# Optimization experiments

Hardware: AMD Instinct MI355X
Metric: run time of the kernel (lower is better)

The kernel has to match this reference:

```python
import jax, jax.numpy as jnp
import numpy as np

B, T, D, E, F, K = 1, 8192, 1024, 8, 4096, 2
CAP_FACTOR = 1.25
AUX_COEFF = 0.01


def setup_inputs() -> dict:
    key = jax.random.key(0)
    k0, k1, k2, k3, k4 = jax.random.split(key, 5)
    x = jax.random.normal(k0, (B, T, D), dtype=jnp.float32)
    Wr = jax.random.normal(k1, (E, D), dtype=jnp.float32) * 0.01  # router, std=0.01 per init
    s = 0.02
    Wg = jax.random.normal(k2, (E, F, D), dtype=jnp.float32) * s  # gate_proj per expert
    Wu = jax.random.normal(k3, (E, F, D), dtype=jnp.float32) * s  # up_proj per expert
    Wd = jax.random.normal(k4, (E, D, F), dtype=jnp.float32) * s  # down_proj per expert
    return {"x": x, "Wr": Wr, "Wg": Wg, "Wu": Wu, "Wd": Wd}


def reference(x, Wr, Wg, Wu, Wd):
    b, t, d = x.shape
    N = b * t
    capacity = max(int(t * K * CAP_FACTOR / E), 1)  # static, matches compute_capacity
    x_flat = x.reshape(N, d)

    # --- router ---
    logits = x_flat @ Wr.T                              # (N, E)
    probs = jax.nn.softmax(logits, axis=-1)
    topw_raw, topi = jax.lax.top_k(probs, K)            # (N, K)
    topw = topw_raw / (topw_raw.sum(-1, keepdims=True) + 1e-9)

    # --- dispatch order: slot-major (slot 0 over all tokens, then slot 1, ...) ---
    flat_e = topi.T.reshape(-1)                         # (K*N,) expert id per assignment
    flat_w = topw.T.reshape(-1)                         # (K*N,)
    tok = jnp.tile(jnp.arange(N), K)                    # (K*N,) token id per assignment

    oh = jax.nn.one_hot(flat_e, E, dtype=jnp.int32)     # (K*N, E)
    rank = (jnp.cumsum(oh, axis=0) - oh)[jnp.arange(K * N), flat_e]  # arrival rank per expert
    accepted = rank < capacity                          # dispatch_mask (slot-major flat)
    pos = jnp.where(accepted, rank, 0)
    dest = flat_e * capacity + pos                      # slot in flattened capacity buffer
    acc_f = accepted.astype(x.dtype)[:, None]

    # scatter tokens into capacity buffers (dropped tokens add zeros)
    buf = jnp.zeros((E * capacity, d), x.dtype).at[dest].add(x_flat[tok] * acc_f)
    expert_in = buf.reshape(E, capacity, d)

    # --- per-expert SwiGLU FFN (batched grouped GEMM) ---
    gate = jax.nn.silu(jnp.einsum('ecd,efd->ecf', expert_in, Wg))
    up = jnp.einsum('ecd,efd->ecf', expert_in, Wu)
    expert_out = jnp.einsum('ecf,edf->ecd', gate * up, Wd).reshape(E * capacity, d)

    # --- weighted combine back to token positions ---
    contrib = flat_w[:, None] * acc_f * expert_out[dest]
    out_flat = jnp.zeros((N, d), x.dtype).at[tok].add(contrib)
    output = out_flat.reshape(b, t, d)

    # --- load-balance aux loss ---
    counts = jnp.zeros(E, x.dtype).at[flat_e].add(accepted.astype(x.dtype))
    total = jnp.maximum(accepted.sum().astype(x.dtype), 1.0)
    f_i = counts / total
    P_i = probs.mean(0)
    aux_loss = AUX_COEFF * E * jnp.sum(f_i * P_i)
    return output, aux_loss
```

## Files before the change

### kernel.cpp

```cpp
#include <hip/hip_runtime.h>
#include <hip/hip_bf16.h>

#define N_TOK 8192
#define DIM   1024
#define NEXP  8
#define FF    4096
#define CAP   2560
#define NASSIGN (N_TOK * 2)

typedef __bf16 bf16;
typedef __bf16 bf16x8 __attribute__((ext_vector_type(8)));
typedef __bf16 bf16x4v __attribute__((ext_vector_type(4)));
typedef float  f32x4  __attribute__((ext_vector_type(4)));

__device__ __forceinline__ void gl2lds16(const bf16* g, bf16* l) {
    __builtin_amdgcn_global_load_lds(
        (const __attribute__((address_space(1))) unsigned int*)g,
        (__attribute__((address_space(3))) unsigned int*)l,
        16, 0, 0);
}

template <int NT>
__device__ __forceinline__ void gemm256_core(
    const bf16* __restrict__ gA, size_t astep,
    const bf16* __restrict__ gB, size_t bstep,
    bf16* As, bf16* Bs, f32x4 acc[8][4], int wave, int lane)
{
    const int wm = wave >> 2, wn = wave & 3;
    const int r16 = lane & 15, c16 = lane >> 4;

    auto STAGE = [&](int kt) {
        const int b = kt & 1;
        const bf16* a  = gA + kt * 64;
        const bf16* bb = gB + kt * 64;
#pragma unroll
        for (int g = 0; g < 4; ++g)
            gl2lds16(a + (size_t)g * astep, &As[b * (256 * 64) + (g * 64 + wave * 8) * 64]);
#pragma unroll
        for (int g = 0; g < 4; ++g)
            gl2lds16(bb + (size_t)g * bstep, &Bs[b * (256 * 64) + (g * 64 + wave * 8) * 64]);
    };

    STAGE(0);
    STAGE(1);

    bf16x8 af[4][2], bfr[2][2];

    for (int kt = 0; kt < NT; ++kt) {
        if (kt < NT - 1) asm volatile("s_waitcnt vmcnt(8)" ::: "memory");
        else             asm volatile("s_waitcnt vmcnt(0)" ::: "memory");
        __builtin_amdgcn_sched_barrier(0);
        __builtin_amdgcn_s_barrier();
        __builtin_amdgcn_sched_barrier(0);
        const bf16* Asb = &As[(kt & 1) * (256 * 64)];
        const bf16* Bsb = &Bs[(kt & 1) * (256 * 64)];

#define DS_A(mh)                                                          \
        _Pragma("unroll")                                                 \
        for (int m = 0; m < 4; ++m) {                                     \
            _Pragma("unroll")                                             \
            for (int kk = 0; kk < 2; ++kk) {                              \
                int row = wm * 128 + (mh) * 64 + m * 16 + r16;            \
                int phys = (kk * 4 + c16) ^ (row & 7);                    \
                af[m][kk] = *(const bf16x8*)&Asb[row * 64 + phys * 8];    \
            } }
#define DS_B(nh)                                                          \
        _Pragma("unroll")                                                 \
        for (int n = 0; n < 2; ++n) {                                     \
            _Pragma("unroll")                                             \
            for (int kk = 0; kk < 2; ++kk) {                              \
                int row = wn * 64 + ((nh) * 2 + n) * 16 + r16;            \
                int phys = (kk * 4 + c16) ^ (row & 7);                    \
                bfr[n][kk] = *(const bf16x8*)&Bsb[row * 64 + phys * 8];   \
            } }
#define PH_IN                                                             \
        __builtin_amdgcn_sched_barrier(0);                                \
        __builtin_amdgcn_s_barrier();                                     \
        asm volatile("s_waitcnt lgkmcnt(0)" ::: "memory");                \
        __builtin_amdgcn_sched_barrier(0);
#define PH_MFMA(mh, nh)                                                   \
        __builtin_amdgcn_s_setprio(1);                                    \
        _Pragma("unroll")                                                 \
        for (int m = 0; m < 4; ++m)                                       \
            _Pragma("unroll")                                             \
            for (int n = 0; n < 2; ++n)                                   \
                _Pragma("unroll")                                         \
                for (int kk = 0; kk < 2; ++kk)                            \
                    acc[(mh) * 4 + m][(nh) * 2 + n] =                     \
                        __builtin_amdgcn_mfma_f32_16x16x32_bf16(          \
                            af[m][kk], bfr[n][kk],                        \
                            acc[(mh) * 4 + m][(nh) * 2 + n], 0, 0, 0);    \
        __builtin_amdgcn_s_setprio(0);
#define PH_OUT                                                            \
        __builtin_amdgcn_sched_barrier(0);                                \
        __builtin_amdgcn_s_barrier();                                     \
        __builtin_amdgcn_sched_barrier(0);

        DS_A(0) DS_B(0) PH_IN PH_MFMA(0, 0) PH_OUT
        DS_B(1)         PH_IN PH_MFMA(0, 1) PH_OUT
        DS_A(1) DS_B(0) PH_IN PH_MFMA(1, 0) PH_OUT
        DS_B(1)         PH_IN PH_MFMA(1, 1) PH_OUT

#undef DS_A
#undef DS_B
#undef PH_IN
#undef PH_MFMA
#undef PH_OUT

        if (kt + 2 < NT) STAGE(kt + 2);
    }
}

__global__ __launch_bounds__(256) void cvt_bf16_kernel(const float* __restrict__ in,
                                                       bf16* __restrict__ out, int n) {
    int stride = gridDim.x * blockDim.x * 8;
    for (int i = (blockIdx.x * blockDim.x + threadIdx.x) * 8; i < n; i += stride) {
        float4 a = *(const float4*)(in + i);
        float4 b = *(const float4*)(in + i + 4);
        bf16x8 o;
        o[0] = (bf16)a.x; o[1] = (bf16)a.y; o[2] = (bf16)a.z; o[3] = (bf16)a.w;
        o[4] = (bf16)b.x; o[5] = (bf16)b.y; o[6] = (bf16)b.z; o[7] = (bf16)b.w;
        *(bf16x8*)(out + i) = o;
    }
}

__global__ __launch_bounds__(256) void router_kernel(const float* __restrict__ x,
                                                     const float* __restrict__ Wr,
                                                     float* __restrict__ probs,
                                                     int* __restrict__ topi,
                                                     float* __restrict__ topw) {
    int wave = threadIdx.x >> 6;
    int lane = threadIdx.x & 63;
    int t = blockIdx.x * 4 + wave;
    const float* xr = x + (size_t)t * DIM;

    double acc[NEXP];
#pragma unroll
    for (int e = 0; e < NEXP; ++e) acc[e] = 0.0;
    for (int i = lane; i < DIM; i += 64) {
        double xv = (double)xr[i];
#pragma unroll
        for (int e = 0; e < NEXP; ++e) acc[e] += xv * (double)Wr[e * DIM + i];
    }
#pragma unroll
    for (int e = 0; e < NEXP; ++e) {
        double v = acc[e];
        for (int off = 32; off > 0; off >>= 1) v += __shfl_down(v, off, 64);
        acc[e] = v;
    }
    if (lane == 0) {
        double mx = acc[0];
        for (int e = 1; e < NEXP; ++e) if (acc[e] > mx) mx = acc[e];
        double p[NEXP], s = 0.0;
        for (int e = 0; e < NEXP; ++e) { p[e] = exp(acc[e] - mx); s += p[e]; }
        float pf[NEXP];
        for (int e = 0; e < NEXP; ++e) { pf[e] = (float)(p[e] / s); probs[t * NEXP + e] = pf[e]; }
        int e1 = 0;
        for (int e = 1; e < NEXP; ++e) if (acc[e] > acc[e1]) e1 = e;
        int e2 = -1;
        for (int e = 0; e < NEXP; ++e) {
            if (e == e1) continue;
            if (e2 < 0 || acc[e] > acc[e2]) e2 = e;
        }
        float w1 = pf[e1], w2 = pf[e2];
        float inv = 1.0f / (w1 + w2 + 1e-9f);
        topi[t * 2 + 0] = e1; topi[t * 2 + 1] = e2;
        topw[t * 2 + 0] = w1 * inv; topw[t * 2 + 1] = w2 * inv;
    }
}

__global__ __launch_bounds__(64) void rank_kernel(const int* __restrict__ topi,
                                                  int* __restrict__ dest,
                                                  int* __restrict__ accf,
                                                  int* __restrict__ counts) {
    int e = blockIdx.x;
    int lane = threadIdx.x;
    const int per = NASSIGN / 64;
    int base = lane * per;
    int cnt = 0;
    for (int i = 0; i < per; ++i) {
        int j = base + i;
        int t = j & (N_TOK - 1), s = j >> 13;
        if (topi[t * 2 + s] == e) cnt++;
    }
    int sum = cnt;
    for (int off = 1; off < 64; off <<= 1) {
        int v = __shfl_up(sum, off, 64);
        if (lane >= off) sum += v;
    }
    int r = sum - cnt;
    int total = __shfl(sum, 63, 64);
    for (int i = 0; i < per; ++i) {
        int j = base + i;
        int t = j & (N_TOK - 1), s = j >> 13;
        if (topi[t * 2 + s] == e) {
            int acc = (r < CAP) ? 1 : 0;
            dest[j] = e * CAP + (acc ? r : 0);
            accf[j] = acc;
            r++;
        }
    }
    if (lane == 63) counts[e] = (total < CAP) ? total : CAP;
}

__global__ __launch_bounds__(256) void gather_kernel(const float* __restrict__ x,
                                                     const int* __restrict__ dest,
                                                     const int* __restrict__ accf,
                                                     bf16* __restrict__ Xe) {
    int j = blockIdx.x;
    if (!accf[j]) return;
    int t = j & (N_TOK - 1);
    int d0 = threadIdx.x * 4;
    float4 v = *(const float4*)(x + (size_t)t * DIM + d0);
    union { bf16 h[4]; uint2 u; } tmp;
    tmp.h[0] = (bf16)v.x; tmp.h[1] = (bf16)v.y; tmp.h[2] = (bf16)v.z; tmp.h[3] = (bf16)v.w;
    *(uint2*)(Xe + (size_t)dest[j] * DIM + d0) = tmp.u;
}

__global__ __launch_bounds__(512, 2) void gateup_kernel(const bf16* __restrict__ Xe,
                                                        const bf16* __restrict__ Wg,
                                                        const bf16* __restrict__ Wu,
                                                        bf16* __restrict__ hbuf) {
    const int e = blockIdx.z;
    const int m0 = blockIdx.x * 256;
    const int n0f = blockIdx.y * 128;
    const int tid = threadIdx.x, lane = tid & 63, wave = tid >> 6;
    const int wm = wave >> 2, wn = wave & 3;
    const int r16 = lane & 15, c16 = lane >> 4;

    __shared__ bf16 As[2 * 256 * 64];
    __shared__ bf16 Bs[2 * 256 * 64];

    const int rsub = wave * 8 + (lane >> 3);
    const int csw  = ((lane & 7) ^ (lane >> 3)) * 8;
    const bf16* gA = Xe + (size_t)e * CAP * DIM + (size_t)(m0 + rsub) * DIM + csw;
    const int bff = n0f + ((rsub >> 5) & 1) * 16 + (rsub & 15);
    const bf16* gB = (((rsub >> 4) & 1) ? Wu : Wg)
                   + (size_t)e * FF * DIM + (size_t)bff * DIM + csw;

    f32x4 acc[8][4] = {};
    gemm256_core<DIM / 64>(gA, (size_t)64 * DIM, gB, (size_t)32 * DIM, As, Bs, acc, wave, lane);

    bf16* hp = hbuf + (size_t)e * CAP * FF;
#pragma unroll
    for (int m = 0; m < 8; ++m)
#pragma unroll
        for (int np = 0; np < 2; ++np)
#pragma unroll
            for (int j = 0; j < 4; ++j) {
                float g = acc[m][2 * np + 0][j];
                float u = acc[m][2 * np + 1][j];
                float h = (g / (1.f + __expf(-g))) * u;
                int gr = m0 + wm * 128 + m * 16 + c16 * 4 + j;
                int gc = n0f + wn * 32 + np * 16 + r16;
                hp[(size_t)gr * FF + gc] = (bf16)h;
            }
}

__global__ __launch_bounds__(512, 2) void down_kernel(const bf16* __restrict__ hbuf,
                                                      const bf16* __restrict__ Wd,
                                                      bf16* __restrict__ eo) {
    const int e  = blockIdx.z >> 1;
    const int kh = blockIdx.z & 1;
    const int m0 = blockIdx.x * 256;
    const int n0 = blockIdx.y * 256;
    const int tid = threadIdx.x, lane = tid & 63, wave = tid >> 6;
    const int wm = wave >> 2, wn = wave & 3;
    const int r16 = lane & 15, c16 = lane >> 4;

    __shared__ bf16 As[2 * 256 * 64];
    __shared__ bf16 Bs[2 * 256 * 64];

    const int rsub = wave * 8 + (lane >> 3);
    const int csw  = ((lane & 7) ^ (lane >> 3)) * 8;
    const bf16* gA = hbuf + (size_t)e * CAP * FF + (size_t)(m0 + rsub) * FF + kh * (FF / 2) + csw;
    const bf16* gB = Wd + (size_t)e * DIM * FF + (size_t)(n0 + rsub) * FF + kh * (FF / 2) + csw;

    f32x4 acc[8][4] = {};
    gemm256_core<FF / 128>(gA, (size_t)64 * FF, gB, (size_t)64 * FF, As, Bs, acc, wave, lane);

    bf16* op = eo + (size_t)kh * NEXP * CAP * DIM + (size_t)e * CAP * DIM;
#pragma unroll
    for (int m = 0; m < 8; ++m)
#pragma unroll
        for (int n = 0; n < 4; ++n)
#pragma unroll
            for (int j = 0; j < 4; ++j) {
                int gr = m0 + wm * 128 + m * 16 + c16 * 4 + j;
                int gc = n0 + wn * 64 + n * 16 + r16;
                op[(size_t)gr * DIM + gc] = (bf16)acc[m][n][j];
            }
}

__global__ __launch_bounds__(256) void combine_kernel(const bf16* __restrict__ eo,
                                                      const int* __restrict__ dest,
                                                      const int* __restrict__ accf,
                                                      const float* __restrict__ topw,
                                                      float* __restrict__ out) {
    int t = blockIdx.x;
    float w0 = accf[t] ? topw[t * 2 + 0] : 0.f;
    float w1 = accf[N_TOK + t] ? topw[t * 2 + 1] : 0.f;
    size_t off1 = (size_t)NEXP * CAP * DIM;
    const bf16* a0 = eo + (size_t)dest[t] * DIM;
    const bf16* b0 = eo + (size_t)dest[N_TOK + t] * DIM;
    int d = threadIdx.x * 4;
    bf16x4v a00 = *(const bf16x4v*)(a0 + d);
    bf16x4v a01 = *(const bf16x4v*)(a0 + off1 + d);
    bf16x4v b00 = *(const bf16x4v*)(b0 + d);
    bf16x4v b01 = *(const bf16x4v*)(b0 + off1 + d);
    float4 o;
    o.x = w0 * ((float)a00[0] + (float)a01[0]) + w1 * ((float)b00[0] + (float)b01[0]);
    o.y = w0 * ((float)a00[1] + (float)a01[1]) + w1 * ((float)b00[1] + (float)b01[1]);
    o.z = w0 * ((float)a00[2] + (float)a01[2]) + w1 * ((float)b00[2] + (float)b01[2]);
    o.w = w0 * ((float)a00[3] + (float)a01[3]) + w1 * ((float)b00[3] + (float)b01[3]);
    *(float4*)(out + (size_t)t * DIM + d) = o;
}

__global__ __launch_bounds__(256) void aux_kernel(const float* __restrict__ probs,
                                                  const int* __restrict__ counts,
                                                  float* __restrict__ out_aux) {
    __shared__ float sm[256][NEXP];
    float loc[NEXP];
#pragma unroll
    for (int e = 0; e < NEXP; ++e) loc[e] = 0.f;
    for (int t = threadIdx.x; t < N_TOK; t += 256)
#pragma unroll
        for (int e = 0; e < NEXP; ++e) loc[e] += probs[t * NEXP + e];
#pragma unroll
    for (int e = 0; e < NEXP; ++e) sm[threadIdx.x][e] = loc[e];
    __syncthreads();
    for (int s = 128; s > 0; s >>= 1) {
        if (threadIdx.x < s)
#pragma unroll
            for (int e = 0; e < NEXP; ++e) sm[threadIdx.x][e] += sm[threadIdx.x + s][e];
        __syncthreads();
    }
    if (threadIdx.x == 0) {
        int tot = 0;
        for (int e = 0; e < NEXP; ++e) tot += counts[e];
        float totf = tot > 0 ? (float)tot : 1.f;
        float aux = 0.f;
        for (int e = 0; e < NEXP; ++e)
            aux += ((float)counts[e] / totf) * (sm[0][e] / (float)N_TOK);
        out_aux[0] = 0.01f * (float)NEXP * aux;
    }
}

extern "C" void kernel_launch(void* const* d_in, const int* in_sizes, int n_in,
                              void* d_out, int out_size, void* d_ws, size_t ws_size,
                              hipStream_t stream) {
    const float* x  = (const float*)d_in[0];
    const float* Wr = (const float*)d_in[1];
    const float* Wg = (const float*)d_in[2];
    const float* Wu = (const float*)d_in[3];
    const float* Wd = (const float*)d_in[4];
    float* out = (float*)d_out;

    char* ws = (char*)d_ws;
    size_t off = 0;
    auto alloc = [&](size_t bytes) -> void* {
        void* p = ws + off;
        off += (bytes + 255) & ~(size_t)255;
        return p;
    };
    const size_t NW = (size_t)NEXP * FF * DIM;
    bf16*  Wg_bf = (bf16*)alloc(NW * sizeof(bf16));
    bf16*  Wu_bf = (bf16*)alloc(NW * sizeof(bf16));
    bf16*  Wd_bf = (bf16*)alloc(NW * sizeof(bf16));
    bf16*  Xe    = (bf16*)alloc((size_t)NEXP * CAP * DIM * sizeof(bf16));
    bf16*  hbuf  = (bf16*)alloc((size_t)NEXP * CAP * FF * sizeof(bf16));
    bf16*  eo    = (bf16*)alloc((size_t)2 * NEXP * CAP * DIM * sizeof(bf16));
    float* probs = (float*)alloc((size_t)N_TOK * NEXP * sizeof(float));
    int*   topi  = (int*)alloc((size_t)N_TOK * 2 * sizeof(int));
    float* topw  = (float*)alloc((size_t)N_TOK * 2 * sizeof(float));
    int*   dst   = (int*)alloc((size_t)NASSIGN * sizeof(int));
    int*   accf  = (int*)alloc((size_t)NASSIGN * sizeof(int));
    int*   cnts  = (int*)alloc(NEXP * sizeof(int));

    cvt_bf16_kernel<<<2048, 256, 0, stream>>>(Wg, Wg_bf, (int)NW);
    cvt_bf16_kernel<<<2048, 256, 0, stream>>>(Wu, Wu_bf, (int)NW);
    cvt_bf16_kernel<<<2048, 256, 0, stream>>>(Wd, Wd_bf, (int)NW);
    router_kernel<<<N_TOK / 4, 256, 0, stream>>>(x, Wr, probs, topi, topw);
    rank_kernel<<<NEXP, 64, 0, stream>>>(topi, dst, accf, cnts);
    gather_kernel<<<NASSIGN, 256, 0, stream>>>(x, dst, accf, Xe);
    gateup_kernel<<<dim3(CAP / 256, FF / 128, NEXP), 512, 0, stream>>>(Xe, Wg_bf, Wu_bf, hbuf);
    down_kernel<<<dim3(CAP / 256, DIM / 256, NEXP * 2), 512, 0, stream>>>(hbuf, Wd_bf, eo);
    combine_kernel<<<N_TOK, 256, 0, stream>>>(eo, dst, accf, topw, out);
    aux_kernel<<<1, 256, 0, stream>>>(probs, cnts, out + (size_t)N_TOK * DIM);
}
```

Before: 1.024 ms.

## Interleave global-to-LDS prefetch into MFMA phases with quarter-tile staging

```diff
diff --git a/kernel.cpp b/kernel.cpp
--- a/kernel.cpp
+++ b/kernel.cpp
@@ -20,95 +20,105 @@
         16, 0, 0);
 }
 
-template <int NT>
+template <int NT, int AST, int BST, int BG1, int BG2>
 __device__ __forceinline__ void gemm256_core(
-    const bf16* __restrict__ gA, size_t astep,
-    const bf16* __restrict__ gB, size_t bstep,
+    const bf16* __restrict__ pA, const bf16* __restrict__ pB,
     bf16* As, bf16* Bs, f32x4 acc[8][4], int wave, int lane)
 {
     const int wm = wave >> 2, wn = wave & 3;
     const int r16 = lane & 15, c16 = lane >> 4;
-
-    auto STAGE = [&](int kt) {
-        const int b = kt & 1;
-        const bf16* a  = gA + kt * 64;
-        const bf16* bb = gB + kt * 64;
-#pragma unroll
-        for (int g = 0; g < 4; ++g)
-            gl2lds16(a + (size_t)g * astep, &As[b * (256 * 64) + (g * 64 + wave * 8) * 64]);
-#pragma unroll
-        for (int g = 0; g < 4; ++g)
-            gl2lds16(bb + (size_t)g * bstep, &Bs[b * (256 * 64) + (g * 64 + wave * 8) * 64]);
-    };
-
-    STAGE(0);
-    STAGE(1);
+    const int wbase = wave * 8 * 64;
+
+#define AOFF(g) ((size_t)(g) * 64 * AST)
+#define BOFF(g) ((size_t)(((g) & 1) * BG1 + ((g) >> 1) * BG2) * BST)
+#define SA(g, kt) gl2lds16(pA + AOFF(g) + (size_t)(kt) * 64, \
+                           &As[((kt) & 1) * (256 * 64) + (g) * (64 * 64) + wbase])
+#define SB(g, kt) gl2lds16(pB + BOFF(g) + (size_t)(kt) * 64, \
+                           &Bs[((kt) & 1) * (256 * 64) + (g) * (64 * 64) + wbase])
+
+    SA(0, 0); SA(2, 0); SB(0, 0); SB(1, 0);
+    SA(1, 0); SA(3, 0); SB(2, 0); SB(3, 0);
+    SA(0, 1); SA(2, 1); SB(0, 1); SB(1, 1);
+    asm volatile("s_waitcnt vmcnt(4)" ::: "memory");
+    __builtin_amdgcn_sched_barrier(0);
+    __builtin_amdgcn_s_barrier();
+    __builtin_amdgcn_sched_barrier(0);
 
     bf16x8 af[4][2], bfr[2][2];
 
-    for (int kt = 0; kt < NT; ++kt) {
-        if (kt < NT - 1) asm volatile("s_waitcnt vmcnt(8)" ::: "memory");
-        else             asm volatile("s_waitcnt vmcnt(0)" ::: "memory");
-        __builtin_amdgcn_sched_barrier(0);
-        __builtin_amdgcn_s_barrier();
-        __builtin_amdgcn_sched_barrier(0);
-        const bf16* Asb = &As[(kt & 1) * (256 * 64)];
-        const bf16* Bsb = &Bs[(kt & 1) * (256 * 64)];
-
-#define DS_A(mh)                                                          \
-        _Pragma("unroll")                                                 \
-        for (int m = 0; m < 4; ++m) {                                     \
-            _Pragma("unroll")                                             \
-            for (int kk = 0; kk < 2; ++kk) {                              \
-                int row = wm * 128 + (mh) * 64 + m * 16 + r16;            \
-                int phys = (kk * 4 + c16) ^ (row & 7);                    \
-                af[m][kk] = *(const bf16x8*)&Asb[row * 64 + phys * 8];    \
-            } }
-#define DS_B(nh)                                                          \
-        _Pragma("unroll")                                                 \
-        for (int n = 0; n < 2; ++n) {                                     \
-            _Pragma("unroll")                                             \
-            for (int kk = 0; kk < 2; ++kk) {                              \
-                int row = wn * 64 + ((nh) * 2 + n) * 16 + r16;            \
-                int phys = (kk * 4 + c16) ^ (row & 7);                    \
-                bfr[n][kk] = *(const bf16x8*)&Bsb[row * 64 + phys * 8];   \
-            } }
-#define PH_IN                                                             \
-        __builtin_amdgcn_sched_barrier(0);                                \
-        __builtin_amdgcn_s_barrier();                                     \
-        asm volatile("s_waitcnt lgkmcnt(0)" ::: "memory");                \
-        __builtin_amdgcn_sched_barrier(0);
-#define PH_MFMA(mh, nh)                                                   \
-        __builtin_amdgcn_s_setprio(1);                                    \
-        _Pragma("unroll")                                                 \
-        for (int m = 0; m < 4; ++m)                                       \
-            _Pragma("unroll")                                             \
-            for (int n = 0; n < 2; ++n)                                   \
-                _Pragma("unroll")                                         \
-                for (int kk = 0; kk < 2; ++kk)                            \
-                    acc[(mh) * 4 + m][(nh) * 2 + n] =                     \
-                        __builtin_amdgcn_mfma_f32_16x16x32_bf16(          \
-                            af[m][kk], bfr[n][kk],                        \
-                            acc[(mh) * 4 + m][(nh) * 2 + n], 0, 0, 0);    \
-        __builtin_amdgcn_s_setprio(0);
-#define PH_OUT                                                            \
-        __builtin_amdgcn_sched_barrier(0);                                \
-        __builtin_amdgcn_s_barrier();                                     \
-        __builtin_amdgcn_sched_barrier(0);
-
-        DS_A(0) DS_B(0) PH_IN PH_MFMA(0, 0) PH_OUT
-        DS_B(1)         PH_IN PH_MFMA(0, 1) PH_OUT
-        DS_A(1) DS_B(0) PH_IN PH_MFMA(1, 0) PH_OUT
-        DS_B(1)         PH_IN PH_MFMA(1, 1) PH_OUT
-
+#define DS_A(mh)                                                           \
+    _Pragma("unroll")                                                      \
+    for (int mm = 0; mm < 4; ++mm) {                                       \
+        _Pragma("unroll")                                                  \
+        for (int kk = 0; kk < 2; ++kk) {                                   \
+            int row = wm * 128 + (mh) * 64 + mm * 16 + r16;                \
+            int phys = (kk * 4 + c16) ^ (row & 7);                         \
+            af[mm][kk] = *(const bf16x8*)&Asb[row * 64 + phys * 8];        \
+        } }
+#define DS_B(nh)                                                           \
+    _Pragma("unroll")                                                      \
+    for (int np = 0; np < 2; ++np) {                                       \
+        _Pragma("unroll")                                                  \
+        for (int kk = 0; kk < 2; ++kk) {                                   \
+            int rl = (nh) * 128 + wn * 32 + np * 16 + r16;                 \
+            int phys = (kk * 4 + c16) ^ (rl & 7);                          \
+            bfr[np][kk] = *(const bf16x8*)&Bsb[rl * 64 + phys * 8];        \
+        } }
+#define PH_IN                                                              \
+    __builtin_amdgcn_sched_barrier(0);                                     \
+    __builtin_amdgcn_s_barrier();                                          \
+    asm volatile("s_waitcnt lgkmcnt(0)" ::: "memory");                     \
+    __builtin_amdgcn_sched_barrier(0);
+#define MFMA16(mh, nh)                                                     \
+    __builtin_amdgcn_s_setprio(1);                                         \
+    _Pragma("unroll")                                                      \
+    for (int mm = 0; mm < 4; ++mm)                                         \
+        _Pragma("unroll")                                                  \
+        for (int np = 0; np < 2; ++np)                                     \
+            _Pragma("unroll")                                              \
+            for (int kk = 0; kk < 2; ++kk)                                 \
+                acc[(mh) * 4 + mm][(nh) * 2 + np] =                        \
+                    __builtin_amdgcn_mfma_f32_16x16x32_bf16(               \
+                        af[mm][kk], bfr[np][kk],                           \
+                        acc[(mh) * 4 + mm][(nh) * 2 + np], 0, 0, 0);       \
+    __builtin_amdgcn_s_setprio(0);
+#define PH_OUT                                                             \
+    __builtin_amdgcn_sched_barrier(0);                                     \
+    __builtin_amdgcn_s_barrier();                                          \
+    __builtin_amdgcn_sched_barrier(0);
+
+#define TILE(kt, S1, S2, VMC) {                                            \
+    const bf16* Asb = &As[((kt) & 1) * (256 * 64)];                        \
+    const bf16* Bsb = &Bs[((kt) & 1) * (256 * 64)];                        \
+    DS_A(0) DS_B(0)                                                        \
+    if (S1) { SA(1, (kt) + 1); SA(3, (kt) + 1); }                          \
+    PH_IN MFMA16(0, 0) PH_OUT                                              \
+    DS_B(1)                                                                \
+    if (S1) { SB(2, (kt) + 1); SB(3, (kt) + 1); }                          \
+    PH_IN MFMA16(0, 1) PH_OUT                                              \
+    DS_A(1) DS_B(0)                                                        \
+    if (S2) { SA(0, (kt) + 2); SA(2, (kt) + 2); }                          \
+    PH_IN MFMA16(1, 0) PH_OUT                                              \
+    DS_B(1)                                                                \
+    if (S2) { SB(0, (kt) + 2); SB(1, (kt) + 2); }                          \
+    if ((VMC) == 4) { asm volatile("s_waitcnt vmcnt(4)" ::: "memory"); }   \
+    else if ((VMC) == 0) { asm volatile("s_waitcnt vmcnt(0)" ::: "memory"); } \
+    PH_IN MFMA16(1, 1) PH_OUT }
+
+    for (int kt = 0; kt < NT - 2; ++kt) TILE(kt, 1, 1, 4);
+    TILE(NT - 2, 1, 0, 0);
+    TILE(NT - 1, 0, 0, -1);
+
+#undef AOFF
+#undef BOFF
+#undef SA
+#undef SB
 #undef DS_A
 #undef DS_B
 #undef PH_IN
-#undef PH_MFMA
+#undef MFMA16
 #undef PH_OUT
-
-        if (kt + 2 < NT) STAGE(kt + 2);
-    }
+#undef TILE
 }
 
 __global__ __launch_bounds__(256) void cvt_bf16_kernel(const float* __restrict__ in,
@@ -231,28 +241,28 @@
     __shared__ bf16 As[2 * 256 * 64];
     __shared__ bf16 Bs[2 * 256 * 64];
 
-    const int rsub = wave * 8 + (lane >> 3);
-    const int csw  = ((lane & 7) ^ (lane >> 3)) * 8;
-    const bf16* gA = Xe + (size_t)e * CAP * DIM + (size_t)(m0 + rsub) * DIM + csw;
-    const int bff = n0f + ((rsub >> 5) & 1) * 16 + (rsub & 15);
-    const bf16* gB = (((rsub >> 4) & 1) ? Wu : Wg)
-                   + (size_t)e * FF * DIM + (size_t)bff * DIM + csw;
+    const int l   = wave * 8 + (lane >> 3);
+    const int csw = ((lane & 7) ^ (lane >> 3)) * 8;
+    const bf16* pA = Xe + (size_t)e * CAP * DIM + (size_t)(m0 + l) * DIM + csw;
+    const int T = (l >> 4) & 1, wnl = l >> 5, r16l = l & 15;
+    const bf16* pB = (T ? Wu : Wg) + (size_t)e * FF * DIM
+                   + (size_t)(n0f + wnl * 32 + r16l) * DIM + csw;
 
     f32x4 acc[8][4] = {};
-    gemm256_core<DIM / 64>(gA, (size_t)64 * DIM, gB, (size_t)32 * DIM, As, Bs, acc, wave, lane);
+    gemm256_core<DIM / 64, DIM, DIM, 64, 16>(pA, pB, As, Bs, acc, wave, lane);
 
     bf16* hp = hbuf + (size_t)e * CAP * FF;
 #pragma unroll
     for (int m = 0; m < 8; ++m)
 #pragma unroll
-        for (int np = 0; np < 2; ++np)
+        for (int cg = 0; cg < 2; ++cg)
 #pragma unroll
             for (int j = 0; j < 4; ++j) {
-                float g = acc[m][2 * np + 0][j];
-                float u = acc[m][2 * np + 1][j];
+                float g = acc[m][cg * 2 + 0][j];
+                float u = acc[m][cg * 2 + 1][j];
                 float h = (g / (1.f + __expf(-g))) * u;
                 int gr = m0 + wm * 128 + m * 16 + c16 * 4 + j;
-                int gc = n0f + wn * 32 + np * 16 + r16;
+                int gc = n0f + wn * 32 + cg * 16 + r16;
                 hp[(size_t)gr * FF + gc] = (bf16)h;
             }
 }
@@ -271,13 +281,17 @@
     __shared__ bf16 As[2 * 256 * 64];
     __shared__ bf16 Bs[2 * 256 * 64];
 
-    const int rsub = wave * 8 + (lane >> 3);
-    const int csw  = ((lane & 7) ^ (lane >> 3)) * 8;
-    const bf16* gA = hbuf + (size_t)e * CAP * FF + (size_t)(m0 + rsub) * FF + kh * (FF / 2) + csw;
-    const bf16* gB = Wd + (size_t)e * DIM * FF + (size_t)(n0 + rsub) * FF + kh * (FF / 2) + csw;
+    const int l   = wave * 8 + (lane >> 3);
+    const int csw = ((lane & 7) ^ (lane >> 3)) * 8;
+    const bf16* pA = hbuf + (size_t)e * CAP * FF + (size_t)(m0 + l) * FF
+                   + kh * (FF / 2) + csw;
+    const int nlow = (l >> 4) & 1, wnl = l >> 5, r16l = l & 15;
+    const bf16* pB = Wd + (size_t)e * DIM * FF
+                   + (size_t)(n0 + wnl * 64 + nlow * 16 + r16l) * FF
+                   + kh * (FF / 2) + csw;
 
     f32x4 acc[8][4] = {};
-    gemm256_core<FF / 128>(gA, (size_t)64 * FF, gB, (size_t)64 * FF, As, Bs, acc, wave, lane);
+    gemm256_core<FF / 128, FF, FF, 128, 32>(pA, pB, As, Bs, acc, wave, lane);
 
     bf16* op = eo + (size_t)kh * NEXP * CAP * DIM + (size_t)e * CAP * DIM;
 #pragma unroll
```

Result: faster. 896.5 us (-12.5%).
